# Kernel tuning notes

Hardware: AMD Instinct MI355X
Metric: run time of the kernel (lower is better)

## Reference

```python
import jax, jax.numpy as jnp
import numpy as np

J = 25
C_IN, HID, LAT = 3, 64, 32


def _graph_conv(x, A, W, b):
    # x: [N,T,J,Cin]; A: [J,J]; W: [Cin,Cout]; b: [Cout]
    A = jax.nn.softmax(A, axis=-1)
    # fused adjacency mix + projection: (A @ x) @ W + b
    x = jnp.einsum('ij,ntjc->ntic', A, x)
    return jnp.einsum('ntjc,cd->ntjd', x, W) + b


def setup_inputs() -> dict:
    key = jax.random.key(0)
    ks = jax.random.split(key, 13)
    x = jax.random.normal(ks[0], (32, 2048, J, C_IN), dtype=jnp.float32)
    eye = jnp.eye(J, dtype=jnp.float32)
    def lin(kw, kb, cin, cout):
        W = jax.random.normal(kw, (cin, cout), dtype=jnp.float32) / np.sqrt(cin)
        b = jax.random.normal(kb, (cout,), dtype=jnp.float32) * 0.01
        return W, b
    W1, b1 = lin(ks[1], ks[2], C_IN, HID)
    W2, b2 = lin(ks[3], ks[4], HID, LAT)
    W3, b3 = lin(ks[5], ks[6], LAT, HID)
    W4, b4 = lin(ks[7], ks[8], HID, C_IN)
    return {
        'x': x,
        'A1': eye, 'W1': W1, 'b1': b1,
        'A2': eye, 'W2': W2, 'b2': b2,
        'A3': eye, 'W3': W3, 'b3': b3,
        'A4': eye, 'W4': W4, 'b4': b4,
    }


def reference(x, A1, W1, b1, A2, W2, b2, A3, W3, b3, A4, W4, b4):
    h = jax.nn.relu(_graph_conv(x, A1, W1, b1))     # encoder_g1 + relu
    z = _graph_conv(h, A2, W2, b2)                  # encoder_g2 (no relu)
    h_dec = jax.nn.relu(_graph_conv(z, A3, W3, b3)) # decoder_g1 + relu
    out = _graph_conv(h_dec, A4, W4, b4)            # decoder_g2
    return out
```

## Files before the change

kernel.cpp:

```cpp
#include <hip/hip_runtime.h>
#include <math.h>

#define J 25
#define NJC 75
#define F 8
#define NTHREADS 512
#define SCRW 2112

#define O_A1T  0
#define O_APP  1024
#define O_A4B  2048
#define O_W2T  3072
#define O_W3T  5120
#define O_W1T  7168
#define O_W4C  8192
#define O_BPP  8448
#define C0_EL  8704
#define C0_U4  1088

using bf16x4 = __attribute__((ext_vector_type(4))) __bf16;
using bf16x8 = __attribute__((ext_vector_type(8))) __bf16;
using f32x4  = __attribute__((ext_vector_type(4))) float;
using f32x16 = __attribute__((ext_vector_type(16))) float;

__device__ inline bf16x8 zero8() {
    bf16x8 z;
    #pragma unroll
    for (int j = 0; j < 8; j++) z[j] = (__bf16)0.f;
    return z;
}

__global__ void gcn_precompute(
    const float* __restrict__ A1, const float* __restrict__ W1, const float* __restrict__ b1,
    const float* __restrict__ A2, const float* __restrict__ W2, const float* __restrict__ b2,
    const float* __restrict__ A3, const float* __restrict__ W3, const float* __restrict__ b3,
    const float* __restrict__ A4, const float* __restrict__ W4, const float* __restrict__ b4,
    __bf16* __restrict__ cw)
{
    __shared__ float T[3125];
    float* T0 = T;        float* T1 = T + 625;  float* T2 = T + 1250;
    float* T3 = T + 1875; float* T4 = T + 2500;
    const int t = threadIdx.x;

    if (t < 100) {
        const int m = t / J, i = t % J;
        const float* Asrc = (m == 0) ? A1 : (m == 1) ? A2 : (m == 2) ? A3 : A4;
        float row[J];
        float mx = -1e30f;
        #pragma unroll
        for (int j = 0; j < J; j++) { row[j] = Asrc[i * J + j]; mx = fmaxf(mx, row[j]); }
        float s = 0.f;
        #pragma unroll
        for (int j = 0; j < J; j++) { row[j] = __expf(row[j] - mx); s += row[j]; }
        const float inv = 1.f / s;
        float* dst = T + m * 625 + i * J;
        #pragma unroll
        for (int j = 0; j < J; j++) dst[j] = row[j] * inv;
    }
    __syncthreads();

    for (int idx = t; idx < 625; idx += 256) {
        const int i = idx / J, jj = idx % J;
        float s = 0.f;
        #pragma unroll
        for (int k = 0; k < J; k++) s += T2[i * J + k] * T1[k * J + jj];
        T4[idx] = s;
    }
    __syncthreads();

    for (int i = t; i < 1024; i += 256) {
        const int b = i >> 8, n = (i >> 3) & 31, jj = i & 7, j = 8 * b + jj;
        const bool ok = (j < J) && (n < J);
        cw[O_A1T + i] = (__bf16)(ok ? T0[n * J + j] : 0.f);
        cw[O_APP + i] = (__bf16)(ok ? T4[n * J + j] : 0.f);
        cw[O_A4B + i] = (__bf16)(ok ? T3[n * J + j] : 0.f);
    }
    for (int i = t; i < 2048; i += 256) {
        const int b = i >> 8, m = (i >> 3) & 31, jj = i & 7;
        cw[O_W2T + i] = (__bf16)W2[(8 * b + jj) * 32 + m];
        const int tt = i >> 10, r = i & 1023;
        const int b3i = r >> 8, m3 = (r >> 3) & 31, j3 = r & 7;
        cw[O_W3T + i] = (__bf16)W3[(8 * b3i + j3) * 64 + tt * 32 + m3];
    }
    for (int i = t; i < 1024; i += 256) {
        const int tt = i >> 9, r = i & 511, hf = r >> 8, q = r & 255;
        const int m = q >> 3, c = q & 7, d = tt * 32 + m;
        float v = 0.f;
        if (hf == 0) {
            if (c < 3) v = W1[c * 64 + d];
            else if (c == 3) v = b1[d];
        }
        cw[O_W1T + i] = (__bf16)v;
    }
    if (t < 256)
        cw[O_W4C + t] = (t < 192) ? (__bf16)W4[(t & 63) * 3 + (t >> 6)] : (__bf16)0.f;

    float* fw = (float*)(cw + O_BPP);
    if (t < 64) {
        float s = b3[t];
        #pragma unroll
        for (int l = 0; l < 32; l++) s += W3[l * 64 + t] * b2[l];
        fw[t] = s;
    }
    if (t >= 64 && t < 68) fw[t] = (t < 67) ? b4[t - 64] : 0.f;
}

__global__ __launch_bounds__(NTHREADS, 6) void gcn_fused(
    const float* __restrict__ x,
    const __bf16* __restrict__ cw,
    float* __restrict__ out, const int NT)
{
    __shared__ __align__(16) __bf16 C0[C0_EL];
    __shared__ __align__(16) __bf16 SCR[F * SCRW];

    const int t = threadIdx.x;

    {
        const uint4* src = (const uint4*)cw;
        uint4* dst = (uint4*)C0;
        for (int i = t; i < C0_U4; i += NTHREADS) dst[i] = src[i];
    }
    __syncthreads();

    const __bf16* A1T  = C0 + O_A1T;
    const __bf16* Appb = C0 + O_APP;
    const __bf16* A4b  = C0 + O_A4B;
    const __bf16* W2T  = C0 + O_W2T;
    const __bf16* W3T  = C0 + O_W3T;
    const __bf16* W1TP = C0 + O_W1T;
    const __bf16* W4c  = C0 + O_W4C;
    const float*  bpps = (const float*)(C0 + O_BPP);
    const float*  b4s  = bpps + 64;

    const int w = t >> 6, lane = t & 63, ln = lane & 31, half = lane >> 5;
    const int f = blockIdx.x * F + w;
    if (f >= NT) return;

    __bf16* sc = &SCR[w * SCRW];

    f32x16 Z;
    #pragma unroll
    for (int z = 0; z < 16; z++) Z[z] = 0.f;

    {
        const int blk = lane >> 4, row = (lane >> 2) & 3, q = (lane & 3) * 2;
        *(unsigned int*)&sc[blk * 264 + row * 8 + q] = 0u;
        if (lane < J) sc[(lane >> 3) * 264 + 24 + (lane & 7)] = (__bf16)1.f;
        for (int i = lane; i < NJC; i += 64) {
            const float v = x[(long)f * NJC + i];
            const int c = i % 3, j = i / 3;
            sc[(j >> 3) * 264 + c * 8 + (j & 7)] = (__bf16)v;
        }
    }

    f32x16 accY;
    {
        bf16x8 a0 = *(const bf16x8*)&sc[(half)*264 + ln * 8];
        bf16x8 b0 = *(const bf16x8*)&A1T[(half)*256 + ln * 8];
        accY = __builtin_amdgcn_mfma_f32_32x32x16_bf16(a0, b0, Z, 0, 0, 0);
        bf16x8 a1 = *(const bf16x8*)&sc[(2 + half) * 264 + ln * 8];
        bf16x8 b1 = *(const bf16x8*)&A1T[(2 + half) * 256 + ln * 8];
        accY = __builtin_amdgcn_mfma_f32_32x32x16_bf16(a1, b1, accY, 0, 0, 0);
    }

    bf16x8 yb;
    #pragma unroll
    for (int jj = 0; jj < 8; jj++)
        yb[jj] = (half == 0 && jj < 4) ? (__bf16)accY[jj] : (__bf16)0.f;
    #pragma unroll
    for (int tt = 0; tt < 2; tt++) {
        bf16x8 a = *(const bf16x8*)&W1TP[tt * 512 + half * 256 + ln * 8];
        f32x16 acc = __builtin_amdgcn_mfma_f32_32x32x16_bf16(a, yb, Z, 0, 0, 0);
        #pragma unroll
        for (int g = 0; g < 4; g++) {
            bf16x4 p;
            #pragma unroll
            for (int r2 = 0; r2 < 4; r2++) p[r2] = (__bf16)fmaxf(acc[4 * g + r2], 0.f);
            *(bf16x4*)&sc[(tt * 4 + g) * 264 + ln * 8 + 4 * half] = p;
        }
    }

    f32x16 accU;
    {
        bf16x8 a0 = *(const bf16x8*)&W2T[half * 256 + ln * 8];
        bf16x8 b0 = *(const bf16x8*)&sc[half * 264 + ln * 8];
        accU = __builtin_amdgcn_mfma_f32_32x32x16_bf16(a0, b0, Z, 0, 0, 0);
        #pragma unroll
        for (int ks = 1; ks < 4; ks++) {
            const int b = half + 2 * ks;
            bf16x8 a  = *(const bf16x8*)&W2T[b * 256 + ln * 8];
            bf16x8 bb = *(const bf16x8*)&sc[b * 264 + ln * 8];
            accU = __builtin_amdgcn_mfma_f32_32x32x16_bf16(a, bb, accU, 0, 0, 0);
        }
    }
    #pragma unroll
    for (int r = 0; r < 16; r++) {
        const int row = (r & 3) + 8 * (r >> 2) + 4 * half;
        sc[(ln >> 3) * 264 + row * 8 + (ln & 7)] = (__bf16)accU[r];
    }

    f32x16 accV;
    {
        bf16x8 a0 = *(const bf16x8*)&Appb[half * 256 + ln * 8];
        bf16x8 b0 = *(const bf16x8*)&sc[half * 264 + ln * 8];
        accV = __builtin_amdgcn_mfma_f32_32x32x16_bf16(a0, b0, Z, 0, 0, 0);
        bf16x8 a1 = *(const bf16x8*)&Appb[(2 + half) * 256 + ln * 8];
        bf16x8 b1 = *(const bf16x8*)&sc[(2 + half) * 264 + ln * 8];
        accV = __builtin_amdgcn_mfma_f32_32x32x16_bf16(a1, b1, accV, 0, 0, 0);
    }
    #pragma unroll
    for (int r = 0; r < 16; r++) {
        const int row = (r & 3) + 8 * (r >> 2) + 4 * half;
        sc[(4 + (ln >> 3)) * 264 + row * 8 + (ln & 7)] = (__bf16)accV[r];
    }

    bf16x8 vb[2];
    #pragma unroll
    for (int ks = 0; ks < 2; ks++)
        vb[ks] = *(const bf16x8*)&sc[(4 + half + 2 * ks) * 264 + ln * 8];
    #pragma unroll
    for (int tt = 0; tt < 2; tt++) {
        bf16x8 a0 = *(const bf16x8*)&W3T[tt * 1024 + half * 256 + ln * 8];
        f32x16 acc = __builtin_amdgcn_mfma_f32_32x32x16_bf16(a0, vb[0], Z, 0, 0, 0);
        bf16x8 a1 = *(const bf16x8*)&W3T[tt * 1024 + (2 + half) * 256 + ln * 8];
        acc = __builtin_amdgcn_mfma_f32_32x32x16_bf16(a1, vb[1], acc, 0, 0, 0);
        #pragma unroll
        for (int g = 0; g < 4; g++) {
            f32x4 bias = *(const f32x4*)&bpps[tt * 32 + 8 * g + 4 * half];
            bf16x4 p;
            #pragma unroll
            for (int r2 = 0; r2 < 4; r2++)
                p[r2] = (__bf16)fmaxf(acc[4 * g + r2] + bias[r2], 0.f);
            *(bf16x4*)&sc[(tt * 4 + g) * 264 + ln * 8 + 4 * half] = p;
        }
    }

    f32x16 accP;
    {
        bf16x8 a0 = *(const bf16x8*)&sc[half * 264 + ln * 8];
        bf16x8 b0 = zero8();
        if (ln < 3) b0 = *(const bf16x8*)&W4c[ln * 64 + half * 8];
        accP = __builtin_amdgcn_mfma_f32_32x32x16_bf16(a0, b0, Z, 0, 0, 0);
        #pragma unroll
        for (int ks = 1; ks < 4; ks++) {
            const int b = half + 2 * ks;
            bf16x8 a = *(const bf16x8*)&sc[b * 264 + ln * 8];
            bf16x8 bb = zero8();
            if (ln < 3) bb = *(const bf16x8*)&W4c[ln * 64 + b * 8];
            accP = __builtin_amdgcn_mfma_f32_32x32x16_bf16(a, bb, accP, 0, 0, 0);
        }
    }
    #pragma unroll
    for (int g = 0; g < 4; g++) {
        bf16x4 p;
        #pragma unroll
        for (int r2 = 0; r2 < 4; r2++) p[r2] = (__bf16)accP[4 * g + r2];
        *(bf16x4*)&sc[g * 264 + ln * 8 + 4 * half] = p;
    }

    f32x16 accO;
    {
        bf16x8 a0 = *(const bf16x8*)&A4b[half * 256 + ln * 8];
        bf16x8 b0 = *(const bf16x8*)&sc[half * 264 + ln * 8];
        accO = __builtin_amdgcn_mfma_f32_32x32x16_bf16(a0, b0, Z, 0, 0, 0);
        bf16x8 a1 = *(const bf16x8*)&A4b[(2 + half) * 256 + ln * 8];
        bf16x8 b1 = *(const bf16x8*)&sc[(2 + half) * 264 + ln * 8];
        accO = __builtin_amdgcn_mfma_f32_32x32x16_bf16(a1, b1, accO, 0, 0, 0);
    }
    if (ln < 3) {
        const float b4v = b4s[ln];
        const long ob = (long)f * NJC;
        #pragma unroll
        for (int r = 0; r < 16; r++) {
            const int row = (r & 3) + 8 * (r >> 2) + 4 * half;
            if (row < J) out[ob + row * 3 + ln] = accO[r] + b4v;
        }
    }
}

extern "C" void kernel_launch(void* const* d_in, const int* in_sizes, int n_in,
                              void* d_out, int out_size, void* d_ws, size_t ws_size,
                              hipStream_t stream)
{
    const float* x  = (const float*)d_in[0];
    const float* A1 = (const float*)d_in[1];
    const float* W1 = (const float*)d_in[2];
    const float* b1 = (const float*)d_in[3];
    const float* A2 = (const float*)d_in[4];
    const float* W2 = (const float*)d_in[5];
    const float* b2 = (const float*)d_in[6];
    const float* A3 = (const float*)d_in[7];
    const float* W3 = (const float*)d_in[8];
    const float* b3 = (const float*)d_in[9];
    const float* A4 = (const float*)d_in[10];
    const float* W4 = (const float*)d_in[11];
    const float* b4 = (const float*)d_in[12];
    float* out = (float*)d_out;
    __bf16* cw = (__bf16*)d_ws;

    const int NT = in_sizes[0] / NJC;
    const int nblocks = (NT + F - 1) / F;

    gcn_precompute<<<1, 256, 0, stream>>>(
        A1, W1, b1, A2, W2, b2, A3, W3, b3, A4, W4, b4, cw);
    gcn_fused<<<nblocks, NTHREADS, 0, stream>>>(x, cw, out, NT);
}
```

Measured before the change: 158.4 us.

## Hold weights in registers and loop each wave over several frames with prefetch

The fused kernel stops staging the constant weights in shared memory per block. Each lane now loads its MFMA weight fragments into registers once, and each wave processes 8 frames in a loop while prefetching the next frame's input. This removes the per-block weight copy and barrier, and it removes the shared-memory reads of weights in every stage. In exchange it raises register pressure and lowers occupancy (256 threads, 3 blocks per CU), and it drops the bounds check, so it assumes NT divides evenly by 32.

```diff
diff --git a/kernel.cpp b/kernel.cpp
--- a/kernel.cpp
+++ b/kernel.cpp
@@ -3,8 +3,9 @@
 
 #define J 25
 #define NJC 75
-#define F 8
-#define NTHREADS 512
+#define NWAVE 4
+#define NTHREADS 256
+#define NFPW 8
 #define SCRW 2112
 
 #define O_A1T  0
@@ -14,13 +15,11 @@
 #define O_W3T  5120
 #define O_W1T  7168
 #define O_W4C  8192
-#define O_BPP  8448
-#define C0_EL  8704
-#define C0_U4  1088
+#define O_BPPB 8448
+#define O_B4   8512
 
 using bf16x4 = __attribute__((ext_vector_type(4))) __bf16;
 using bf16x8 = __attribute__((ext_vector_type(8))) __bf16;
-using f32x4  = __attribute__((ext_vector_type(4))) float;
 using f32x16 = __attribute__((ext_vector_type(16))) float;
 
 __device__ inline bf16x8 zero8() {
@@ -38,6 +37,7 @@
     __bf16* __restrict__ cw)
 {
     __shared__ float T[3125];
+    __shared__ float bpp[64];
     float* T0 = T;        float* T1 = T + 625;  float* T2 = T + 1250;
     float* T3 = T + 1875; float* T4 = T + 2500;
     const int t = threadIdx.x;
@@ -56,6 +56,12 @@
         float* dst = T + m * 625 + i * J;
         #pragma unroll
         for (int j = 0; j < J; j++) dst[j] = row[j] * inv;
+    }
+    if (t < 64) {
+        float s = b3[t];
+        #pragma unroll
+        for (int l = 0; l < 32; l++) s += W3[l * 64 + t] * b2[l];
+        bpp[t] = s;
     }
     __syncthreads();
 
@@ -95,186 +101,198 @@
     if (t < 256)
         cw[O_W4C + t] = (t < 192) ? (__bf16)W4[(t & 63) * 3 + (t >> 6)] : (__bf16)0.f;
 
-    float* fw = (float*)(cw + O_BPP);
     if (t < 64) {
-        float s = b3[t];
-        #pragma unroll
-        for (int l = 0; l < 32; l++) s += W3[l * 64 + t] * b2[l];
-        fw[t] = s;
-    }
-    if (t >= 64 && t < 68) fw[t] = (t < 67) ? b4[t - 64] : 0.f;
+        const int tt = t >> 5, rem = t & 31, hf = rem >> 4, q = rem & 15;
+        const int g = q >> 2, r2 = q & 3;
+        cw[O_BPPB + t] = (__bf16)bpp[tt * 32 + 8 * g + 4 * hf + r2];
+    }
+    float* fb4 = (float*)(cw + O_B4);
+    if (t >= 64 && t < 68) fb4[t - 64] = (t < 67) ? b4[t - 64] : 0.f;
 }
 
-__global__ __launch_bounds__(NTHREADS, 6) void gcn_fused(
+__global__ __launch_bounds__(NTHREADS, 3) void gcn_fused(
     const float* __restrict__ x,
     const __bf16* __restrict__ cw,
-    float* __restrict__ out, const int NT)
+    float* __restrict__ out)
 {
-    __shared__ __align__(16) __bf16 C0[C0_EL];
-    __shared__ __align__(16) __bf16 SCR[F * SCRW];
+    __shared__ __align__(16) __bf16 SCR[NWAVE * SCRW];
 
     const int t = threadIdx.x;
-
-    {
-        const uint4* src = (const uint4*)cw;
-        uint4* dst = (uint4*)C0;
-        for (int i = t; i < C0_U4; i += NTHREADS) dst[i] = src[i];
-    }
-    __syncthreads();
-
-    const __bf16* A1T  = C0 + O_A1T;
-    const __bf16* Appb = C0 + O_APP;
-    const __bf16* A4b  = C0 + O_A4B;
-    const __bf16* W2T  = C0 + O_W2T;
-    const __bf16* W3T  = C0 + O_W3T;
-    const __bf16* W1TP = C0 + O_W1T;
-    const __bf16* W4c  = C0 + O_W4C;
-    const float*  bpps = (const float*)(C0 + O_BPP);
-    const float*  b4s  = bpps + 64;
-
     const int w = t >> 6, lane = t & 63, ln = lane & 31, half = lane >> 5;
-    const int f = blockIdx.x * F + w;
-    if (f >= NT) return;
-
+    const int fo = ln * 8;
     __bf16* sc = &SCR[w * SCRW];
 
+    const long fbase = ((long)blockIdx.x * NWAVE + w) * NFPW;
+
+    long xb = fbase * NJC;
+    float xv0 = x[xb + lane];
+    float xv1 = (lane < NJC - 64) ? x[xb + 64 + lane] : 0.f;
+
+    bf16x8 rA1T[2], rApp[2], rA4b[2], rW1[2], rW2[4], rW3[4], rW4[4], rBpp[4];
+    #pragma unroll
+    for (int ks = 0; ks < 2; ks++) {
+        rA1T[ks] = *(const bf16x8*)&cw[O_A1T + (2 * ks + half) * 256 + fo];
+        rApp[ks] = *(const bf16x8*)&cw[O_APP + (2 * ks + half) * 256 + fo];
+        rA4b[ks] = *(const bf16x8*)&cw[O_A4B + (2 * ks + half) * 256 + fo];
+        rW1[ks]  = *(const bf16x8*)&cw[O_W1T + ks * 512 + half * 256 + fo];
+    }
+    #pragma unroll
+    for (int ks = 0; ks < 4; ks++)
+        rW2[ks] = *(const bf16x8*)&cw[O_W2T + (half + 2 * ks) * 256 + fo];
+    #pragma unroll
+    for (int tt = 0; tt < 2; tt++)
+        #pragma unroll
+        for (int ks = 0; ks < 2; ks++)
+            rW3[tt * 2 + ks] = *(const bf16x8*)&cw[O_W3T + tt * 1024 + (half + 2 * ks) * 256 + fo];
+    #pragma unroll
+    for (int ks = 0; ks < 4; ks++) {
+        rW4[ks] = zero8();
+        if (ln < 3) rW4[ks] = *(const bf16x8*)&cw[O_W4C + ln * 64 + (half + 2 * ks) * 8];
+    }
+    #pragma unroll
+    for (int tt = 0; tt < 2; tt++)
+        #pragma unroll
+        for (int p = 0; p < 2; p++)
+            rBpp[tt * 2 + p] = *(const bf16x8*)&cw[O_BPPB + (tt * 2 + half) * 16 + p * 8];
+    float b4v = 0.f;
+    if (ln < 3) b4v = ((const float*)(cw + O_B4))[ln];
+
     f32x16 Z;
     #pragma unroll
     for (int z = 0; z < 16; z++) Z[z] = 0.f;
 
-    {
-        const int blk = lane >> 4, row = (lane >> 2) & 3, q = (lane & 3) * 2;
-        *(unsigned int*)&sc[blk * 264 + row * 8 + q] = 0u;
-        if (lane < J) sc[(lane >> 3) * 264 + 24 + (lane & 7)] = (__bf16)1.f;
-        for (int i = lane; i < NJC; i += 64) {
-            const float v = x[(long)f * NJC + i];
-            const int c = i % 3, j = i / 3;
-            sc[(j >> 3) * 264 + c * 8 + (j & 7)] = (__bf16)v;
-        }
-    }
-
-    f32x16 accY;
-    {
-        bf16x8 a0 = *(const bf16x8*)&sc[(half)*264 + ln * 8];
-        bf16x8 b0 = *(const bf16x8*)&A1T[(half)*256 + ln * 8];
-        accY = __builtin_amdgcn_mfma_f32_32x32x16_bf16(a0, b0, Z, 0, 0, 0);
-        bf16x8 a1 = *(const bf16x8*)&sc[(2 + half) * 264 + ln * 8];
-        bf16x8 b1 = *(const bf16x8*)&A1T[(2 + half) * 256 + ln * 8];
-        accY = __builtin_amdgcn_mfma_f32_32x32x16_bf16(a1, b1, accY, 0, 0, 0);
-    }
-
-    bf16x8 yb;
-    #pragma unroll
-    for (int jj = 0; jj < 8; jj++)
-        yb[jj] = (half == 0 && jj < 4) ? (__bf16)accY[jj] : (__bf16)0.f;
-    #pragma unroll
-    for (int tt = 0; tt < 2; tt++) {
-        bf16x8 a = *(const bf16x8*)&W1TP[tt * 512 + half * 256 + ln * 8];
-        f32x16 acc = __builtin_amdgcn_mfma_f32_32x32x16_bf16(a, yb, Z, 0, 0, 0);
+    for (int fi = 0; fi < NFPW; fi++) {
+        const long f = fbase + fi;
+
+        {
+            const int i0 = lane, c0 = i0 % 3, j0 = i0 / 3;
+            sc[(j0 >> 3) * 264 + c0 * 8 + (j0 & 7)] = (__bf16)xv0;
+            if (lane < NJC - 64) {
+                const int i1 = 64 + lane, c1 = i1 % 3, j1 = i1 / 3;
+                sc[(j1 >> 3) * 264 + c1 * 8 + (j1 & 7)] = (__bf16)xv1;
+            }
+            if (half == 0) sc[(ln >> 3) * 264 + 24 + (ln & 7)] = (ln < J) ? (__bf16)1.f : (__bf16)0.f;
+            if (lane < 21) sc[3 * 264 + (lane / 7) * 8 + 1 + (lane % 7)] = (__bf16)0.f;
+        }
+
+        float nxv0 = 0.f, nxv1 = 0.f;
+        if (fi + 1 < NFPW) {
+            const long nxb = (f + 1) * NJC;
+            nxv0 = x[nxb + lane];
+            if (lane < NJC - 64) nxv1 = x[nxb + 64 + lane];
+        }
+
+        f32x16 accY;
+        {
+            bf16x8 a0 = *(const bf16x8*)&sc[half * 264 + fo];
+            accY = __builtin_amdgcn_mfma_f32_32x32x16_bf16(a0, rA1T[0], Z, 0, 0, 0);
+            bf16x8 a1 = *(const bf16x8*)&sc[(2 + half) * 264 + fo];
+            accY = __builtin_amdgcn_mfma_f32_32x32x16_bf16(a1, rA1T[1], accY, 0, 0, 0);
+        }
+
+        bf16x8 yb;
+        #pragma unroll
+        for (int jj = 0; jj < 8; jj++)
+            yb[jj] = (half == 0 && jj < 4) ? (__bf16)accY[jj] : (__bf16)0.f;
+        #pragma unroll
+        for (int tt = 0; tt < 2; tt++) {
+            f32x16 acc = __builtin_amdgcn_mfma_f32_32x32x16_bf16(rW1[tt], yb, Z, 0, 0, 0);
+            #pragma unroll
+            for (int g = 0; g < 4; g++) {
+                bf16x4 p;
+                #pragma unroll
+                for (int r2 = 0; r2 < 4; r2++) p[r2] = (__bf16)fmaxf(acc[4 * g + r2], 0.f);
+                *(bf16x4*)&sc[(tt * 4 + g) * 264 + fo + 4 * half] = p;
+            }
+        }
+
+        f32x16 accU;
+        {
+            bf16x8 a0 = *(const bf16x8*)&sc[half * 264 + fo];
+            accU = __builtin_amdgcn_mfma_f32_32x32x16_bf16(a0, rW2[0], Z, 0, 0, 0);
+            #pragma unroll
+            for (int ks = 1; ks < 4; ks++) {
+                bf16x8 a = *(const bf16x8*)&sc[(half + 2 * ks) * 264 + fo];
+                accU = __builtin_amdgcn_mfma_f32_32x32x16_bf16(a, rW2[ks], accU, 0, 0, 0);
+            }
+        }
         #pragma unroll
         for (int g = 0; g < 4; g++) {
             bf16x4 p;
             #pragma unroll
-            for (int r2 = 0; r2 < 4; r2++) p[r2] = (__bf16)fmaxf(acc[4 * g + r2], 0.f);
-            *(bf16x4*)&sc[(tt * 4 + g) * 264 + ln * 8 + 4 * half] = p;
-        }
-    }
-
-    f32x16 accU;
-    {
-        bf16x8 a0 = *(const bf16x8*)&W2T[half * 256 + ln * 8];
-        bf16x8 b0 = *(const bf16x8*)&sc[half * 264 + ln * 8];
-        accU = __builtin_amdgcn_mfma_f32_32x32x16_bf16(a0, b0, Z, 0, 0, 0);
-        #pragma unroll
-        for (int ks = 1; ks < 4; ks++) {
-            const int b = half + 2 * ks;
-            bf16x8 a  = *(const bf16x8*)&W2T[b * 256 + ln * 8];
-            bf16x8 bb = *(const bf16x8*)&sc[b * 264 + ln * 8];
-            accU = __builtin_amdgcn_mfma_f32_32x32x16_bf16(a, bb, accU, 0, 0, 0);
-        }
-    }
-    #pragma unroll
-    for (int r = 0; r < 16; r++) {
-        const int row = (r & 3) + 8 * (r >> 2) + 4 * half;
-        sc[(ln >> 3) * 264 + row * 8 + (ln & 7)] = (__bf16)accU[r];
-    }
-
-    f32x16 accV;
-    {
-        bf16x8 a0 = *(const bf16x8*)&Appb[half * 256 + ln * 8];
-        bf16x8 b0 = *(const bf16x8*)&sc[half * 264 + ln * 8];
-        accV = __builtin_amdgcn_mfma_f32_32x32x16_bf16(a0, b0, Z, 0, 0, 0);
-        bf16x8 a1 = *(const bf16x8*)&Appb[(2 + half) * 256 + ln * 8];
-        bf16x8 b1 = *(const bf16x8*)&sc[(2 + half) * 264 + ln * 8];
-        accV = __builtin_amdgcn_mfma_f32_32x32x16_bf16(a1, b1, accV, 0, 0, 0);
-    }
-    #pragma unroll
-    for (int r = 0; r < 16; r++) {
-        const int row = (r & 3) + 8 * (r >> 2) + 4 * half;
-        sc[(4 + (ln >> 3)) * 264 + row * 8 + (ln & 7)] = (__bf16)accV[r];
-    }
-
-    bf16x8 vb[2];
-    #pragma unroll
-    for (int ks = 0; ks < 2; ks++)
-        vb[ks] = *(const bf16x8*)&sc[(4 + half + 2 * ks) * 264 + ln * 8];
-    #pragma unroll
-    for (int tt = 0; tt < 2; tt++) {
-        bf16x8 a0 = *(const bf16x8*)&W3T[tt * 1024 + half * 256 + ln * 8];
-        f32x16 acc = __builtin_amdgcn_mfma_f32_32x32x16_bf16(a0, vb[0], Z, 0, 0, 0);
-        bf16x8 a1 = *(const bf16x8*)&W3T[tt * 1024 + (2 + half) * 256 + ln * 8];
-        acc = __builtin_amdgcn_mfma_f32_32x32x16_bf16(a1, vb[1], acc, 0, 0, 0);
+            for (int r2 = 0; r2 < 4; r2++) p[r2] = (__bf16)accU[4 * g + r2];
+            *(bf16x4*)&sc[g * 264 + fo + 4 * half] = p;
+        }
+
+        f32x16 accV;
+        {
+            bf16x8 a0 = *(const bf16x8*)&sc[half * 264 + fo];
+            accV = __builtin_amdgcn_mfma_f32_32x32x16_bf16(a0, rApp[0], Z, 0, 0, 0);
+            bf16x8 a1 = *(const bf16x8*)&sc[(2 + half) * 264 + fo];
+            accV = __builtin_amdgcn_mfma_f32_32x32x16_bf16(a1, rApp[1], accV, 0, 0, 0);
+        }
         #pragma unroll
         for (int g = 0; g < 4; g++) {
-            f32x4 bias = *(const f32x4*)&bpps[tt * 32 + 8 * g + 4 * half];
             bf16x4 p;
             #pragma unroll
-            for (int r2 = 0; r2 < 4; r2++)
-                p[r2] = (__bf16)fmaxf(acc[4 * g + r2] + bias[r2], 0.f);
-            *(bf16x4*)&sc[(tt * 4 + g) * 264 + ln * 8 + 4 * half] = p;
-        }
-    }
-
-    f32x16 accP;
-    {
-        bf16x8 a0 = *(const bf16x8*)&sc[half * 264 + ln * 8];
-        bf16x8 b0 = zero8();
-        if (ln < 3) b0 = *(const bf16x8*)&W4c[ln * 64 + half * 8];
-        accP = __builtin_amdgcn_mfma_f32_32x32x16_bf16(a0, b0, Z, 0, 0, 0);
-        #pragma unroll
-        for (int ks = 1; ks < 4; ks++) {
-            const int b = half + 2 * ks;
-            bf16x8 a = *(const bf16x8*)&sc[b * 264 + ln * 8];
-            bf16x8 bb = zero8();
-            if (ln < 3) bb = *(const bf16x8*)&W4c[ln * 64 + b * 8];
-            accP = __builtin_amdgcn_mfma_f32_32x32x16_bf16(a, bb, accP, 0, 0, 0);
-        }
-    }
-    #pragma unroll
-    for (int g = 0; g < 4; g++) {
-        bf16x4 p;
-        #pragma unroll
-        for (int r2 = 0; r2 < 4; r2++) p[r2] = (__bf16)accP[4 * g + r2];
-        *(bf16x4*)&sc[g * 264 + ln * 8 + 4 * half] = p;
-    }
-
-    f32x16 accO;
-    {
-        bf16x8 a0 = *(const bf16x8*)&A4b[half * 256 + ln * 8];
-        bf16x8 b0 = *(const bf16x8*)&sc[half * 264 + ln * 8];
-        accO = __builtin_amdgcn_mfma_f32_32x32x16_bf16(a0, b0, Z, 0, 0, 0);
-        bf16x8 a1 = *(const bf16x8*)&A4b[(2 + half) * 256 + ln * 8];
-        bf16x8 b1 = *(const bf16x8*)&sc[(2 + half) * 264 + ln * 8];
-        accO = __builtin_amdgcn_mfma_f32_32x32x16_bf16(a1, b1, accO, 0, 0, 0);
-    }
-    if (ln < 3) {
-        const float b4v = b4s[ln];
-        const long ob = (long)f * NJC;
-        #pragma unroll
-        for (int r = 0; r < 16; r++) {
-            const int row = (r & 3) + 8 * (r >> 2) + 4 * half;
-            if (row < J) out[ob + row * 3 + ln] = accO[r] + b4v;
-        }
+            for (int r2 = 0; r2 < 4; r2++) p[r2] = (__bf16)accV[4 * g + r2];
+            *(bf16x4*)&sc[(4 + g) * 264 + fo + 4 * half] = p;
+        }
+
+        bf16x8 vb0 = *(const bf16x8*)&sc[(4 + half) * 264 + fo];
+        bf16x8 vb1 = *(const bf16x8*)&sc[(6 + half) * 264 + fo];
+        #pragma unroll
+        for (int tt = 0; tt < 2; tt++) {
+            f32x16 acc = __builtin_amdgcn_mfma_f32_32x32x16_bf16(rW3[tt * 2 + 0], vb0, Z, 0, 0, 0);
+            acc = __builtin_amdgcn_mfma_f32_32x32x16_bf16(rW3[tt * 2 + 1], vb1, acc, 0, 0, 0);
+            #pragma unroll
+            for (int g = 0; g < 4; g++) {
+                bf16x4 p;
+                #pragma unroll
+                for (int r2 = 0; r2 < 4; r2++) {
+                    const int q = g * 4 + r2;
+                    const float bias = (float)rBpp[tt * 2 + (q >> 3)][q & 7];
+                    p[r2] = (__bf16)fmaxf(acc[4 * g + r2] + bias, 0.f);
+                }
+                *(bf16x4*)&sc[(tt * 4 + g) * 264 + fo + 4 * half] = p;
+            }
+        }
+
+        f32x16 accP;
+        {
+            bf16x8 a0 = *(const bf16x8*)&sc[half * 264 + fo];
+            accP = __builtin_amdgcn_mfma_f32_32x32x16_bf16(a0, rW4[0], Z, 0, 0, 0);
+            #pragma unroll
+            for (int ks = 1; ks < 4; ks++) {
+                bf16x8 a = *(const bf16x8*)&sc[(half + 2 * ks) * 264 + fo];
+                accP = __builtin_amdgcn_mfma_f32_32x32x16_bf16(a, rW4[ks], accP, 0, 0, 0);
+            }
+        }
+        #pragma unroll
+        for (int g = 0; g < 4; g++) {
+            bf16x4 p;
+            #pragma unroll
+            for (int r2 = 0; r2 < 4; r2++) p[r2] = (__bf16)accP[4 * g + r2];
+            *(bf16x4*)&sc[g * 264 + fo + 4 * half] = p;
+        }
+
+        f32x16 accO;
+        {
+            bf16x8 b0 = *(const bf16x8*)&sc[half * 264 + fo];
+            accO = __builtin_amdgcn_mfma_f32_32x32x16_bf16(rA4b[0], b0, Z, 0, 0, 0);
+            bf16x8 b1 = *(const bf16x8*)&sc[(2 + half) * 264 + fo];
+            accO = __builtin_amdgcn_mfma_f32_32x32x16_bf16(rA4b[1], b1, accO, 0, 0, 0);
+        }
+        if (ln < 3) {
+            const long ob = f * NJC;
+            #pragma unroll
+            for (int r = 0; r < 16; r++) {
+                const int row = (r & 3) + 8 * (r >> 2) + 4 * half;
+                if (row < J) out[ob + row * 3 + ln] = accO[r] + b4v;
+            }
+        }
+
+        xv0 = nxv0; xv1 = nxv1;
     }
 }
 
@@ -299,9 +317,9 @@
     __bf16* cw = (__bf16*)d_ws;
 
     const int NT = in_sizes[0] / NJC;
-    const int nblocks = (NT + F - 1) / F;
+    const int nblocks = NT / (NWAVE * NFPW);
 
     gcn_precompute<<<1, 256, 0, stream>>>(
         A1, W1, b1, A2, W2, b2, A3, W3, b3, A4, W4, b4, cw);
-    gcn_fused<<<nblocks, NTHREADS, 0, stream>>>(x, cw, out, NT);
+    gcn_fused<<<nblocks, NTHREADS, 0, stream>>>(x, cw, out);
 }
```

Measured after the change: 153.7 us. 3.0% less time.
